# Kernel tuning notes

Hardware: AMD Instinct MI355X
Metric: run time of the kernel (lower is better)

## Reference

```python
import jax, jax.numpy as jnp
import numpy as np

NUM_HEADS = 16
EMBED_DIM = 1024
HEAD_DIM = EMBED_DIM // NUM_HEADS


def _rel_shift(r):
    # r: (B, tlen, rlen). Pad with ONES (faithful to original), shift, tril.
    B, tlen, rlen = r.shape
    pad = jnp.ones((B, tlen, 1), dtype=r.dtype)
    rp = jnp.concatenate([pad, r], axis=2).reshape(B, rlen + 1, tlen)
    return jnp.tril(rp[:, 1:, :].reshape(B, tlen, rlen))


def setup_inputs() -> dict:
    key = jax.random.key(0)
    ks = jax.random.split(key, 12)
    T, B, E, H, D = 128, 8, EMBED_DIM, NUM_HEADS, HEAD_DIM
    query = jax.random.normal(ks[0], (T, B, E), dtype=jnp.float32)
    key_t = jax.random.normal(ks[1], (T, B, E), dtype=jnp.float32)
    value = jax.random.normal(ks[2], (T, B, E), dtype=jnp.float32)
    rel_pe = jax.random.normal(ks[3], (T, B, E), dtype=jnp.float32)
    # causal mask: True = masked (future positions)
    causal = ~jnp.tril(jnp.ones((T, T), dtype=bool))
    attn_mask = jnp.broadcast_to(causal, (B * H, T, T))
    utt_mask = jnp.ones((B * H, T, T, 1), dtype=jnp.float32)
    spk_mask = jax.random.randint(ks[4], (B, T, T), 0, 2, dtype=jnp.int32)
    s = 1.0 / np.sqrt(E)
    q_w = jax.random.uniform(ks[5], (E, E), jnp.float32, -s, s)
    k_w = jax.random.uniform(ks[6], (E, E), jnp.float32, -s, s)
    v_w = jax.random.uniform(ks[7], (E, E), jnp.float32, -s, s)
    r_w = jax.random.uniform(ks[8], (E, E), jnp.float32, -s, s)
    spk_emb = jax.random.uniform(ks[9], (2, E), jnp.float32, -s, s)
    out_w = jax.random.uniform(ks[10], (E, E), jnp.float32, -s, s)
    return {"query": query, "key": key_t, "value": value, "rel_pe": rel_pe,
            "attn_mask": attn_mask, "utt_mask": utt_mask, "spk_mask": spk_mask,
            "q_w": q_w, "k_w": k_w, "v_w": v_w, "r_w": r_w,
            "spk_emb": spk_emb, "out_w": out_w}


def reference(query, key, value, rel_pe, attn_mask, utt_mask, spk_mask,
              q_w, k_w, v_w, r_w, spk_emb, out_w):
    T, B, E = query.shape
    H, D = NUM_HEADS, HEAD_DIM
    scaling = float(D) ** -0.5

    def split_heads(x):  # (T, B, E) -> (B*H, T, D)
        return x.reshape(T, B * H, D).transpose(1, 0, 2)

    # NOTE: original computes k and v from `query` (faithful)
    q = split_heads(query @ q_w.T)
    k = split_heads(query @ k_w.T)
    v = split_heads(query @ v_w.T)
    r = split_heads(rel_pe @ r_w.T)

    # s_q: speaker embedding row 0 broadcast to all positions
    s_q = split_heads(jnp.broadcast_to(spk_emb[0], (T, B, E)))
    # s_k: (B, T, T, E) -> (B*H, T, T, D), same reshape chain as original
    s_k = spk_emb[spk_mask]                                   # (B, T, T, E)
    s_k = s_k.reshape(B, T * T, E).transpose(1, 0, 2)         # (T*T, B, E)
    s_k = s_k.reshape(T * T, B * H, D).transpose(1, 0, 2)     # (B*H, T*T, D)
    s_k = s_k.reshape(B * H, T, T, D) * utt_mask              # (B*H, T, T, D)

    new_q = q + s_q
    a1 = jnp.einsum('nid,njd->nij', new_q, k)
    a2 = jnp.einsum('nid,nijd->nij', new_q, s_k)
    a3 = _rel_shift(jnp.einsum('nid,njd->nij', s_q, r))

    w = (a1 + a2 + a3) * scaling
    w = jnp.where(attn_mask, jnp.asarray(1e-30, w.dtype), w)
    w = jax.nn.softmax(w, axis=-1)

    out = jnp.einsum('nij,njd->nid', w, v)                    # (B*H, T, D)
    out = out.transpose(1, 0, 2).reshape(T, B, E) @ out_w.T
    return out
```

## Files before the change

### kernel.cpp

```cpp
#include <hip/hip_runtime.h>
#include <hip/hip_bf16.h>
#include <cstddef>
#include <cstdint>


typedef _Float16 f16;
typedef __attribute__((ext_vector_type(8))) _Float16 f16x8;
typedef __attribute__((ext_vector_type(4))) float f32x4;

#define GLOBAL_TO_LDS(g, l) __builtin_amdgcn_global_load_lds( \
    (const __attribute__((address_space(1))) void*)(g),       \
    (__attribute__((address_space(3))) void*)(l), 16, 0, 0)

struct Ptr7 { const float* s[7]; };

__global__ __launch_bounds__(256) void tof16_kernel(Ptr7 p, f16* dbase)
{
    const float* s = p.s[blockIdx.y];
    f16* d = dbase + (size_t)blockIdx.y * (1u << 20);
    const int i = (blockIdx.x * 256 + threadIdx.x) * 8;
    const float4 a = *(const float4*)(s + i);
    const float4 b = *(const float4*)(s + i + 4);
    f16x8 o;
    o[0] = (f16)a.x; o[1] = (f16)a.y; o[2] = (f16)a.z; o[3] = (f16)a.w;
    o[4] = (f16)b.x; o[5] = (f16)b.y; o[6] = (f16)b.z; o[7] = (f16)b.w;
    *(f16x8*)(d + i) = o;
}

template <int TM, int TN, class Epi>
__device__ __forceinline__ void gemm2ph(const f16* __restrict__ A,
                                        const f16* __restrict__ B,
                                        int kbeg, int kend, int m0, int n0,
                                        Epi epi)
{
    constexpr int AITS = TM / 32, BITS = TN / 32;
    constexpr int FM = TM / 32, FN = TN / 32;
    __shared__ __attribute__((aligned(16))) f16 As0[TM * 64];
    __shared__ __attribute__((aligned(16))) f16 As1[TM * 64];
    __shared__ __attribute__((aligned(16))) f16 Bs0[TN * 64];
    __shared__ __attribute__((aligned(16))) f16 Bs1[TN * 64];
    const int tid = threadIdx.x;
    const int wave = tid >> 6, lane = tid & 63;
    const int wr = wave >> 1, wc = wave & 1;
    const int l16 = lane & 15, lk = lane >> 4;
    f32x4 acc[FM][FN] = {};

    auto stage = [&](f16* as_, f16* bs_, int k0) {
#pragma unroll
        for (int it = 0; it < AITS; ++it) {
            const int ebase = it * 2048 + wave * 512;
            const int e = ebase + lane * 8;
            const int row = e >> 6, slot = (e >> 3) & 7;
            const int scol = (slot ^ (row & 7)) << 3;
            GLOBAL_TO_LDS(A + (size_t)(m0 + row) * 1024 + k0 + scol, as_ + ebase);
        }
#pragma unroll
        for (int it = 0; it < BITS; ++it) {
            const int ebase = it * 2048 + wave * 512;
            const int e = ebase + lane * 8;
            const int row = e >> 6, slot = (e >> 3) & 7;
            const int scol = (slot ^ (row & 7)) << 3;
            GLOBAL_TO_LDS(B + (size_t)(n0 + row) * 1024 + k0 + scol, bs_ + ebase);
        }
    };
    auto compute = [&](const f16* as_, const f16* bs_) {
#pragma unroll
        for (int ksl = 0; ksl < 2; ++ksl) {
            const int s = ksl * 4 + lk;
            f16x8 af[FM], bg[FN];
#pragma unroll
            for (int mi = 0; mi < FM; ++mi) {
                const int r = wr * (TM / 2) + mi * 16 + l16;
                af[mi] = *(const f16x8*)(as_ + r * 64 + ((s ^ (r & 7)) << 3));
            }
#pragma unroll
            for (int ni = 0; ni < FN; ++ni) {
                const int r = wc * (TN / 2) + ni * 16 + l16;
                bg[ni] = *(const f16x8*)(bs_ + r * 64 + ((s ^ (r & 7)) << 3));
            }
#pragma unroll
            for (int mi = 0; mi < FM; ++mi)
#pragma unroll
                for (int ni = 0; ni < FN; ++ni)
                    acc[mi][ni] = __builtin_amdgcn_mfma_f32_16x16x32_f16(
                        af[mi], bg[ni], acc[mi][ni], 0, 0, 0);
        }
    };

    const int NT = (kend - kbeg) >> 6;
    stage(As0, Bs0, kbeg);
    __syncthreads();
    int k0 = kbeg;
    for (int t = 0; t < NT; t += 2) {
        if (t + 1 < NT) stage(As1, Bs1, k0 + 64);
        compute(As0, Bs0);
        __syncthreads();
        if (t + 2 < NT) stage(As0, Bs0, k0 + 128);
        compute(As1, Bs1);
        __syncthreads();
        k0 += 128;
    }
#pragma unroll
    for (int mi = 0; mi < FM; ++mi)
#pragma unroll
        for (int ni = 0; ni < FN; ++ni)
#pragma unroll
            for (int r = 0; r < 4; ++r)
                epi(m0 + wr * (TM / 2) + mi * 16 + lk * 4 + r,
                    n0 + wc * (TN / 2) + ni * 16 + l16, acc[mi][ni][r]);
}

struct EpiHead {
    f16* dst; const float* addvec;
    __device__ void operator()(int row, int col, float v) const {
        const float x = addvec ? v + addvec[col] : v;
        const int b = row & 7, t = row >> 3, h = col >> 6, d = col & 63;
        dst[(size_t)(((b << 4) + h) * 128 + t) * 64 + d] = (f16)x;
    }
};
struct EpiF32 {
    float* dst;
    __device__ void operator()(int row, int col, float v) const {
        dst[(size_t)row * 1024 + col] = v;
    }
};

__global__ __launch_bounds__(256) void proj4_kernel(
    const f16* __restrict__ qf, const f16* __restrict__ rf,
    const f16* __restrict__ wbase, const float* __restrict__ spk_emb,
    f16* __restrict__ Qh, f16* __restrict__ Kh,
    f16* __restrict__ Vh, f16* __restrict__ Rh)
{
    const int bid = blockIdx.x;
    const int z = (bid & 7) >> 1;
    const int w = ((bid >> 3) << 1) | (bid & 1);
    const int m0 = (w >> 3) << 6;
    const int n0 = (w & 7) << 7;
    const f16* A = (z == 3) ? rf : qf;
    const f16* W = wbase + ((size_t)z << 20);
    f16* dst = (z == 0) ? Qh : (z == 1) ? Kh : (z == 2) ? Vh : Rh;
    EpiHead epi{dst, (z == 0) ? spk_emb : nullptr};
    gemm2ph<64, 128>(A, W, 0, 1024, m0, n0, epi);
}

__global__ __launch_bounds__(256) void out_kernel(
    const f16* __restrict__ ATT, const f16* __restrict__ owf,
    float* __restrict__ P0, float* __restrict__ P1)
{
    const int bid = blockIdx.x;
    const int g = bid & 7;
    const int kz = g >> 2;
    const int w = ((bid >> 3) << 2) + (g & 3);
    const int m0 = (w >> 3) << 6;
    const int n0 = (w & 7) << 7;
    EpiF32 epi{kz ? P1 : P0};
    gemm2ph<64, 128>(ATT, owf, kz * 512, kz * 512 + 512, m0, n0, epi);
}

__global__ __launch_bounds__(256) void addreduce_kernel(
    const float* __restrict__ a, const float* __restrict__ b, float* __restrict__ o)
{
    const int i = (blockIdx.x * 256 + threadIdx.x) * 4;
    const float4 x = *(const float4*)(a + i);
    const float4 y = *(const float4*)(b + i);
    *(float4*)(o + i) = make_float4(x.x + y.x, x.y + y.y, x.z + y.z, x.w + y.w);
}

__global__ __launch_bounds__(256) void attn_mfma_kernel(
    const f16* __restrict__ Qh, const f16* __restrict__ Kh,
    const f16* __restrict__ Vh, const f16* __restrict__ Rh,
    const float* __restrict__ spk_emb, const int* __restrict__ spk_mask,
    const float* __restrict__ utt_mask, f16* __restrict__ ATT)
{
    __shared__ __attribute__((aligned(16))) char smem[58880];
    f16* nq = (f16*)smem;
    f16* kt = (f16*)(smem + 8192);
    f16* vt = (f16*)(smem + 24576);
    f16* vs = (f16*)(smem + 40960);
    float* cbuf = (float*)(smem + 57344);
    float* dd   = (float*)(smem + 57856);
    float* sq   = (float*)(smem + 58368);

    const int bx = blockIdx.x, n = bx >> 1, half = bx & 1;
    const int b = n >> 4, h = n & 15, i0 = half << 6;
    const int tid = threadIdx.x, wave = tid >> 6, lane = tid & 63;
    const int l16 = lane & 15, lk = lane >> 4;
    const size_t hb = (size_t)n * (128 * 64);

    if (tid < 128)
        sq[tid] = spk_emb[(tid >> 6) * 1024 + (h << 6) + (tid & 63)];

#pragma unroll
    for (int it = 0; it < 2; ++it) {
        const int ebase = it * 2048 + wave * 512;
        const int e = ebase + lane * 8;
        const int row = e >> 6, slot = (e >> 3) & 7;
        const int scol = (slot ^ (row & 7)) << 3;
        GLOBAL_TO_LDS(Qh + hb + (size_t)(i0 + row) * 64 + scol, nq + ebase);
    }
#pragma unroll
    for (int it = 0; it < 4; ++it) {
        const int ebase = it * 2048 + wave * 512;
        const int e = ebase + lane * 8;
        const int row = e >> 6, slot = (e >> 3) & 7;
        const int scol = (slot ^ (row & 7)) << 3;
        GLOBAL_TO_LDS(Kh + hb + (size_t)row * 64 + scol, kt + ebase);
        GLOBAL_TO_LDS(Vh + hb + (size_t)row * 64 + scol, vs + ebase);
    }
    __syncthreads();

    {
        const int st = tid >> 1, hf = tid & 1;
        const int jt = st & 15, dt = st >> 4;
        f16x8 v[8];
#pragma unroll
        for (int jj = 0; jj < 8; ++jj) {
            const int j = jt * 8 + jj;
            v[jj] = *(const f16x8*)(vs + j * 64 + ((dt ^ (j & 7)) << 3));
        }
#pragma unroll
        for (int dr = 0; dr < 4; ++dr) {
            f16x8 w;
            int d;
            if (hf == 0) {
                d = dt * 8 + dr;
#pragma unroll
                for (int jj = 0; jj < 8; ++jj) w[jj] = v[jj][dr];
            } else {
                d = dt * 8 + 4 + dr;
#pragma unroll
                for (int jj = 0; jj < 8; ++jj) w[jj] = v[jj][4 + dr];
            }
            *(f16x8*)(vt + d * 128 + ((jt ^ (d & 7)) << 3)) = w;
        }
    }

    if (tid < 128) {
        const int j = tid;
        float s = 0.f;
#pragma unroll
        for (int c = 0; c < 8; ++c) {
            const f16x8 rv = *(const f16x8*)(Rh + hb + (size_t)j * 64 + c * 8);
#pragma unroll
            for (int e = 0; e < 8; ++e)
                s = fmaf((float)rv[e], sq[c * 8 + e], s);
        }
        cbuf[j] = s;
    } else if (tid < 192) {
        const int i = tid - 128;
        float s0 = 0.f, s1 = 0.f;
#pragma unroll
        for (int c = 0; c < 8; ++c) {
            const f16x8 qv = *(const f16x8*)(nq + i * 64 + ((c ^ (i & 7)) << 3));
#pragma unroll
            for (int e = 0; e < 8; ++e) {
                const float q = (float)qv[e];
                s0 = fmaf(q, sq[c * 8 + e], s0);
                s1 = fmaf(q, sq[64 + c * 8 + e], s1);
            }
        }
        dd[i] = s0; dd[64 + i] = s1;
    }
    __syncthreads();

    const int iw = wave * 16 + l16;
    f16x8 af[2];
#pragma unroll
    for (int ksl = 0; ksl < 2; ++ksl) {
        const int s = ksl * 4 + lk;
        af[ksl] = *(const f16x8*)(nq + iw * 64 + ((s ^ (iw & 7)) << 3));
    }
    f32x4 sacc[8] = {};
#pragma unroll
    for (int ksl = 0; ksl < 2; ++ksl) {
        const int s = ksl * 4 + lk;
#pragma unroll
        for (int ni = 0; ni < 8; ++ni) {
            const int j = ni * 16 + l16;
            const f16x8 bg = *(const f16x8*)(kt + j * 64 + ((s ^ (j & 7)) << 3));
            sacc[ni] = __builtin_amdgcn_mfma_f32_16x16x32_f16(af[ksl], bg, sacc[ni], 0, 0, 0);
        }
    }

    const int il0 = wave * 16 + lk * 4;
    float sc[8][4];
#pragma unroll
    for (int ni = 0; ni < 8; ++ni) {
        const int j = ni * 16 + l16;
#pragma unroll
        for (int r = 0; r < 4; ++r) {
            const int il = il0 + r, i = i0 + il;
            const float du = utt_mask[((size_t)n * 128 + i) * 128 + j];
            const int   sm = spk_mask[((size_t)b * 128 + i) * 128 + j];
            const float a2 = du * (sm ? dd[64 + il] : dd[il]);
            const float a3 = (j <= i) ? cbuf[127 - i + j] : 0.f;
            const float v = (sacc[ni][r] + a2 + a3) * 0.125f;
            sc[ni][r] = (j > i) ? 1e-30f : v;
        }
    }
    float inv[4];
    f16* ps = vs + wave * 2048;
#pragma unroll
    for (int r = 0; r < 4; ++r) {
        float m = sc[0][r];
#pragma unroll
        for (int ni = 1; ni < 8; ++ni) m = fmaxf(m, sc[ni][r]);
#pragma unroll
        for (int off = 8; off > 0; off >>= 1) m = fmaxf(m, __shfl_xor(m, off, 64));
        float ssum = 0.f;
#pragma unroll
        for (int ni = 0; ni < 8; ++ni) {
            const float e = __expf(sc[ni][r] - m);
            sc[ni][r] = e;
            ssum += e;
        }
#pragma unroll
        for (int off = 8; off > 0; off >>= 1) ssum += __shfl_xor(ssum, off, 64);
        inv[r] = 1.f / ssum;
    }
#pragma unroll
    for (int ni = 0; ni < 8; ++ni) {
        const int j = ni * 16 + l16;
#pragma unroll
        for (int r = 0; r < 4; ++r) {
            const int il = lk * 4 + r;
            ps[il * 128 + ((((j >> 3) ^ (il & 7)) << 3) | (j & 7))] = (f16)sc[ni][r];
        }
    }

    f16x8 pa[4];
#pragma unroll
    for (int ks = 0; ks < 4; ++ks) {
        const int slot = ks * 4 + lk;
        pa[ks] = *(const f16x8*)(ps + l16 * 128 + ((slot ^ (l16 & 7)) << 3));
    }
    f32x4 oacc[4] = {};
#pragma unroll
    for (int ks = 0; ks < 4; ++ks) {
        const int slot = ks * 4 + lk;
#pragma unroll
        for (int nd = 0; nd < 4; ++nd) {
            const int d = nd * 16 + l16;
            const f16x8 vb = *(const f16x8*)(vt + d * 128 + ((slot ^ (d & 7)) << 3));
            oacc[nd] = __builtin_amdgcn_mfma_f32_16x16x32_f16(pa[ks], vb, oacc[nd], 0, 0, 0);
        }
    }
#pragma unroll
    for (int nd = 0; nd < 4; ++nd)
#pragma unroll
        for (int r = 0; r < 4; ++r) {
            const int i = i0 + il0 + r;
            const int col = (h << 6) + nd * 16 + l16;
            ATT[(size_t)(i * 8 + b) * 1024 + col] = (f16)(oacc[nd][r] * inv[r]);
        }
}

extern "C" void kernel_launch(void* const* d_in, const int* in_sizes, int n_in,
                              void* d_out, int out_size, void* d_ws, size_t ws_size,
                              hipStream_t stream)
{
    (void)in_sizes; (void)n_in; (void)out_size; (void)ws_size;

    const float* query  = (const float*)d_in[0];
    const float* rel_pe = (const float*)d_in[3];
    const float* utt    = (const float*)d_in[5];
    const int*   spk    = (const int*)d_in[6];
    const float* qw     = (const float*)d_in[7];
    const float* kw     = (const float*)d_in[8];
    const float* vw     = (const float*)d_in[9];
    const float* rw     = (const float*)d_in[10];
    const float* spke   = (const float*)d_in[11];
    const float* ow     = (const float*)d_in[12];

    char* ws = (char*)d_ws;
    f16* Qh  = (f16*)(ws);
    f16* Kh  = (f16*)(ws + (2u  << 20));
    f16* Vh  = (f16*)(ws + (4u  << 20));
    f16* Rh  = (f16*)(ws + (6u  << 20));
    f16* ATT = (f16*)(ws + (8u  << 20));
    f16* fb  = (f16*)(ws + (10u << 20));
    float* P0 = (float*)(ws + (24u << 20));
    float* P1 = (float*)(ws + (28u << 20));

    f16* qf = fb;
    f16* rf = fb + (1u << 20);
    f16* wb = fb + (2u << 20);
    f16* ob = fb + (6u << 20);

    Ptr7 p7;
    p7.s[0] = query; p7.s[1] = rel_pe; p7.s[2] = qw; p7.s[3] = kw;
    p7.s[4] = vw; p7.s[5] = rw; p7.s[6] = ow;

    tof16_kernel<<<dim3(512, 7), 256, 0, stream>>>(p7, fb);
    proj4_kernel<<<dim3(512), 256, 0, stream>>>(qf, rf, wb, spke, Qh, Kh, Vh, Rh);
    attn_mfma_kernel<<<dim3(256), 256, 0, stream>>>(Qh, Kh, Vh, Rh, spke, spk, utt, ATT);
    out_kernel<<<dim3(256), 256, 0, stream>>>(ATT, ob, P0, P1);
    addreduce_kernel<<<dim3(1024), 256, 0, stream>>>(P0, P1, (float*)d_out);
}
```

Before: 54.60 us.

## Triple-buffer GEMM pipeline with vmcnt waits and drop split-K output reduction

Replaces the double-buffered GEMM mainloop with a three-stage LDS ring that issues loads two tiles ahead. Each stage waits with a partial s_waitcnt vmcnt plus a barrier instead of a full __syncthreads, so more async global-to-LDS copies stay in flight. The output projection changes from split-K into two fp32 partial buffers plus a separate add kernel to 32-row tiles over the full K, writing the output directly. This removes one launch and the partial-buffer traffic, at the cost of more LDS per block and a loop hardcoded to K=1024.

```diff
diff --git a/kernel.cpp b/kernel.cpp
--- a/kernel.cpp
+++ b/kernel.cpp
@@ -11,6 +11,12 @@
 #define GLOBAL_TO_LDS(g, l) __builtin_amdgcn_global_load_lds( \
     (const __attribute__((address_space(1))) void*)(g),       \
     (__attribute__((address_space(3))) void*)(l), 16, 0, 0)
+
+#define PIPE_SYNC(N) do {                                      \
+    asm volatile("s_waitcnt vmcnt(" #N ")" ::: "memory");      \
+    __builtin_amdgcn_s_barrier();                              \
+    __builtin_amdgcn_sched_barrier(0);                         \
+} while (0)
 
 struct Ptr7 { const float* s[7]; };
 
@@ -28,17 +34,19 @@
 }
 
 template <int TM, int TN, class Epi>
-__device__ __forceinline__ void gemm2ph(const f16* __restrict__ A,
+__device__ __forceinline__ void gemm3ph(const f16* __restrict__ A,
                                         const f16* __restrict__ B,
-                                        int kbeg, int kend, int m0, int n0,
-                                        Epi epi)
+                                        int m0, int n0, Epi epi)
 {
     constexpr int AITS = TM / 32, BITS = TN / 32;
+    constexpr int LD = AITS + BITS;
     constexpr int FM = TM / 32, FN = TN / 32;
     __shared__ __attribute__((aligned(16))) f16 As0[TM * 64];
     __shared__ __attribute__((aligned(16))) f16 As1[TM * 64];
+    __shared__ __attribute__((aligned(16))) f16 As2[TM * 64];
     __shared__ __attribute__((aligned(16))) f16 Bs0[TN * 64];
     __shared__ __attribute__((aligned(16))) f16 Bs1[TN * 64];
+    __shared__ __attribute__((aligned(16))) f16 Bs2[TN * 64];
     const int tid = threadIdx.x;
     const int wave = tid >> 6, lane = tid & 63;
     const int wr = wave >> 1, wc = wave & 1;
@@ -86,20 +94,29 @@
                         af[mi], bg[ni], acc[mi][ni], 0, 0, 0);
         }
     };
-
-    const int NT = (kend - kbeg) >> 6;
-    stage(As0, Bs0, kbeg);
-    __syncthreads();
-    int k0 = kbeg;
-    for (int t = 0; t < NT; t += 2) {
-        if (t + 1 < NT) stage(As1, Bs1, k0 + 64);
+    auto sync_steady = [&]() {
+        if constexpr (LD == 6) PIPE_SYNC(6); else PIPE_SYNC(5);
+    };
+
+    stage(As0, Bs0, 0);
+    stage(As1, Bs1, 64);
+    int k = 0;
+#pragma unroll 1
+    for (int t = 0; t < 15; t += 3) {
+        sync_steady();
+        if (t + 2 < 16) stage(As2, Bs2, k + 128);
         compute(As0, Bs0);
-        __syncthreads();
-        if (t + 2 < NT) stage(As0, Bs0, k0 + 128);
+        sync_steady();
+        if (t + 3 < 16) stage(As0, Bs0, k + 192);
         compute(As1, Bs1);
-        __syncthreads();
-        k0 += 128;
-    }
+        sync_steady();
+        if (t + 4 < 16) stage(As1, Bs1, k + 256);
+        compute(As2, Bs2);
+        k += 192;
+    }
+    PIPE_SYNC(0);
+    compute(As0, Bs0);
+
 #pragma unroll
     for (int mi = 0; mi < FM; ++mi)
 #pragma unroll
@@ -140,30 +157,18 @@
     const f16* W = wbase + ((size_t)z << 20);
     f16* dst = (z == 0) ? Qh : (z == 1) ? Kh : (z == 2) ? Vh : Rh;
     EpiHead epi{dst, (z == 0) ? spk_emb : nullptr};
-    gemm2ph<64, 128>(A, W, 0, 1024, m0, n0, epi);
+    gemm3ph<64, 128>(A, W, m0, n0, epi);
 }
 
 __global__ __launch_bounds__(256) void out_kernel(
     const f16* __restrict__ ATT, const f16* __restrict__ owf,
-    float* __restrict__ P0, float* __restrict__ P1)
+    float* __restrict__ out)
 {
     const int bid = blockIdx.x;
-    const int g = bid & 7;
-    const int kz = g >> 2;
-    const int w = ((bid >> 3) << 2) + (g & 3);
-    const int m0 = (w >> 3) << 6;
-    const int n0 = (w & 7) << 7;
-    EpiF32 epi{kz ? P1 : P0};
-    gemm2ph<64, 128>(ATT, owf, kz * 512, kz * 512 + 512, m0, n0, epi);
-}
-
-__global__ __launch_bounds__(256) void addreduce_kernel(
-    const float* __restrict__ a, const float* __restrict__ b, float* __restrict__ o)
-{
-    const int i = (blockIdx.x * 256 + threadIdx.x) * 4;
-    const float4 x = *(const float4*)(a + i);
-    const float4 y = *(const float4*)(b + i);
-    *(float4*)(o + i) = make_float4(x.x + y.x, x.y + y.y, x.z + y.z, x.w + y.w);
+    const int m0 = (bid >> 3) << 5;
+    const int n0 = (bid & 7) << 7;
+    EpiF32 epi{out};
+    gemm3ph<32, 128>(ATT, owf, m0, n0, epi);
 }
 
 __global__ __launch_bounds__(256) void attn_mfma_kernel(
@@ -379,8 +384,6 @@
     f16* Rh  = (f16*)(ws + (6u  << 20));
     f16* ATT = (f16*)(ws + (8u  << 20));
     f16* fb  = (f16*)(ws + (10u << 20));
-    float* P0 = (float*)(ws + (24u << 20));
-    float* P1 = (float*)(ws + (28u << 20));
 
     f16* qf = fb;
     f16* rf = fb + (1u << 20);
@@ -394,6 +397,5 @@
     tof16_kernel<<<dim3(512, 7), 256, 0, stream>>>(p7, fb);
     proj4_kernel<<<dim3(512), 256, 0, stream>>>(qf, rf, wb, spke, Qh, Kh, Vh, Rh);
     attn_mfma_kernel<<<dim3(256), 256, 0, stream>>>(Qh, Kh, Vh, Rh, spke, spk, utt, ATT);
-    out_kernel<<<dim3(256), 256, 0, stream>>>(ATT, ob, P0, P1);
-    addreduce_kernel<<<dim3(1024), 256, 0, stream>>>(P0, P1, (float*)d_out);
-}
+    out_kernel<<<dim3(256), 256, 0, stream>>>(ATT, ob, (float*)d_out);
+}
```

Result: faster. 51.35 us (-5.9%).
